# Kernel optimization log

Hardware: AMD Instinct MI355X
Metric: run time of the kernel (lower is better)

Reference implementation:

```python
import jax, jax.numpy as jnp
import numpy as np
import math

DIM = 256
HEADS = 8
HID = DIM * HEADS


def mish(x):
    return x * jnp.tanh(jax.nn.softplus(x))


def setup_inputs() -> dict:
    key = jax.random.key(0)
    ks = jax.random.split(key, 12)
    b, t, l = 4, 16, 256
    s = 1.0 / math.sqrt(DIM)
    inp = {
        "qkv_x": jax.random.normal(ks[0], (b, t, l, DIM), jnp.float32),
        "t_embed": jax.random.normal(ks[1], (b, t, 1, DIM), jnp.float32),
        "reward_embed": jax.random.normal(ks[2], (b, t, 1, DIM), jnp.float32),
        "Wq": jax.random.normal(ks[3], (DIM, HID), jnp.float32) * s,
        "Wk": jax.random.normal(ks[4], (DIM, HID), jnp.float32) * s,
        "Wv": jax.random.normal(ks[5], (DIM, HID), jnp.float32) * s,
        "Wq_t": jax.random.normal(ks[6], (DIM, HID), jnp.float32) * s,
        "bq_t": jnp.zeros((HID,), jnp.float32),
        "Wk_t": jax.random.normal(ks[7], (DIM, HID), jnp.float32) * s,
        "bk_t": jnp.zeros((HID,), jnp.float32),
        "Wv_t": jax.random.normal(ks[8], (DIM, HID), jnp.float32) * s,
        "bv_t": jnp.zeros((HID,), jnp.float32),
        "Wo": jax.random.normal(ks[9], (HID, DIM), jnp.float32) * (1.0 / math.sqrt(HID)),
        "bo": jnp.zeros((DIM,), jnp.float32),
    }
    return inp


def reference(qkv_x, t_embed, reward_embed, Wq, Wk, Wv, Wq_t, bq_t, Wk_t, bk_t, Wv_t, bv_t, Wo, bo):
    b, t, l, f = qkv_x.shape
    x = qkv_x.reshape(b * t, l, f)                    # (bt, l, f)
    tr = (t_embed + reward_embed).reshape(b * t, 1, f)  # (bt, 1, f)
    m = mish(tr)

    def proj(W, Wt, bt_):
        # bias-add of time-conditioning broadcast over l, split heads
        y = x @ W + (m @ Wt + bt_)                    # (bt, l, H*D)
        return y.reshape(b * t, l, HEADS, DIM).transpose(0, 2, 1, 3)  # (bt, H, l, D)

    q = proj(Wq, Wq_t, bq_t)
    k = proj(Wk, Wk_t, bk_t)
    v = proj(Wv, Wv_t, bv_t)

    scores = jnp.einsum('bhqd,bhkd->bhqk', q, k) / math.sqrt(DIM)
    attn = jax.nn.softmax(scores, axis=-1)
    out = jnp.einsum('bhqk,bhkd->bhqd', attn, v)      # (bt, H, l, D)
    out = out.transpose(0, 2, 1, 3).reshape(b, t, l, HEADS * DIM)
    return out @ Wo + bo
```

## Files before the change

kernel.cpp:

```cpp
#include <hip/hip_runtime.h>
#include <stdint.h>

typedef __bf16 bf16x8 __attribute__((ext_vector_type(8)));
typedef float f32x4 __attribute__((ext_vector_type(4)));
typedef uint32_t u32x4 __attribute__((ext_vector_type(4)));

#define MFMA16(a,b,c) __builtin_amdgcn_mfma_f32_16x16x32_bf16(a,b,c,0,0,0)

#define OFF_XB   0ull
#define OFF_WT   8388608ull
#define OFF_WTT  11534336ull
#define OFF_WOT  14680064ull
#define OFF_MB   15728640ull
#define OFF_BIAS 15761408ull
#define OFF_K    17334272ull
#define OFF_VT   84443136ull
#define WS_NEED  151552000ull
#define OFF_Q    151552000ull
#define WS_NEED2 218660864ull

__device__ __forceinline__ uint16_t f2bf(float f) {
  uint32_t u = __builtin_bit_cast(uint32_t, f);
  return (uint16_t)((u + 0x7fffu + ((u >> 16) & 1u)) >> 16);
}
__device__ __forceinline__ bf16x8 ld16(const uint16_t* p) {
  u32x4 v = *(const u32x4*)p;
  return __builtin_bit_cast(bf16x8, v);
}
__device__ __forceinline__ void gll16(const uint16_t* g, char* l) {
  __builtin_amdgcn_global_load_lds(
      (const __attribute__((address_space(1))) void*)g,
      (__attribute__((address_space(3))) void*)l, 16, 0, 0);
}
__device__ __forceinline__ void bounce_w2(char* slab, int row, int col, uint16_t val) {
  int slot = col >> 3;
  *(uint16_t*)(slab + row * 256 + (((slot ^ (row & 7)) & 15) << 4) + ((col & 7) << 1)) = val;
}
__device__ __forceinline__ bf16x8 bounce_r16(const char* slab, int row, int slot) {
  u32x4 v = *(const u32x4*)(slab + row * 256 + (((slot ^ (row & 7)) & 15) << 4));
  return __builtin_bit_cast(bf16x8, v);
}

__global__ void sentinel_kernel(float* out, float val) {
  out[blockIdx.x * 256 + threadIdx.x] = val;
}
__global__ void init_out(const float* bo, float* out) {
  int i = blockIdx.x * 256 + threadIdx.x;
  out[i] = bo[i & 255];
}

__global__ void mish_kernel(const float* te, const float* re, uint16_t* mb) {
  int i = blockIdx.x * 256 + threadIdx.x;
  float x = te[i] + re[i];
  float sp = log1pf(__expf(x));
  mb[i] = f2bf(x * tanhf(sp));
}

__global__ void convx_kernel(const float* x, uint16_t* xb) {
  int i = blockIdx.x * 256 + threadIdx.x;
  float4 v = ((const float4*)x)[i];
  ushort4 o = make_ushort4(f2bf(v.x), f2bf(v.y), f2bf(v.z), f2bf(v.w));
  ((ushort4*)xb)[i] = o;
}

__global__ void wtrans_kernel(const float* w0, const float* w1, const float* w2,
                              const float* w3, const float* w4, const float* w5,
                              const float* w6, uint16_t* wt, uint16_t* wtt, uint16_t* wot) {
  int z = blockIdx.y;
  const float* src; uint16_t* dst; int C;
  if (z < 3)      { src = (z==0)?w0:((z==1)?w1:w2); dst = wt  + (size_t)z*524288;     C=2048; }
  else if (z < 6) { src = (z==3)?w3:((z==4)?w4:w5); dst = wtt + (size_t)(z-3)*524288; C=2048; }
  else            { src = w6; dst = wot;                                              C=256; }
  int R = (z < 6) ? 256 : 2048;
  __shared__ uint16_t tile[32][33];
  int tc = C >> 5;
  int bR = (blockIdx.x / tc) << 5, bC = (blockIdx.x % tc) << 5;
  int tx = threadIdx.x & 31, ty = threadIdx.x >> 5;
  #pragma unroll
  for (int i = 0; i < 4; i++) {
    int r = bR + ty + i * 8;
    tile[ty + i * 8][tx] = f2bf(src[(size_t)r * C + bC + tx]);
  }
  __syncthreads();
  #pragma unroll
  for (int i = 0; i < 4; i++) {
    int c = bC + ty + i * 8;
    dst[(size_t)c * R + bR + tx] = tile[tx][ty + i * 8];
  }
}

__global__ __launch_bounds__(256, 4)
void bias_gemm(const uint16_t* Mb, const uint16_t* WTT,
               const float* bq, const float* bk, const float* bv, float* biasAll) {
  int bid = blockIdx.x;
  int z = bid >> 4, nbt = bid & 15;
  int n0 = nbt << 7;
  const uint16_t* Bsrc = WTT + (size_t)z * 524288;
  const float* bvec = (z == 0) ? bq : ((z == 1) ? bk : bv);
  float* outp = biasAll + (size_t)z * 131072;
  int tid = threadIdx.x, lane = tid & 63, w = tid >> 6;
  int g = lane >> 4, ln = lane & 15;

  bf16x8 af[8];
  #pragma unroll
  for (int ks = 0; ks < 8; ks++)
    af[ks] = ld16(Mb + (size_t)(w*16 + ln) * 256 + ks*32 + g*8);
  f32x4 acc[8];
  #pragma unroll
  for (int j = 0; j < 8; j++) acc[j] = (f32x4){0.f,0.f,0.f,0.f};
  #pragma unroll
  for (int j = 0; j < 8; j++)
    #pragma unroll
    for (int ks = 0; ks < 8; ks++) {
      bf16x8 bf_ = ld16(Bsrc + (size_t)(n0 + j*16 + ln) * 256 + ks*32 + g*8);
      acc[j] = MFMA16(af[ks], bf_, acc[j]);
    }
  #pragma unroll
  for (int j = 0; j < 8; j++) {
    int colg = n0 + j*16 + ln;
    float bb = bvec[colg];
    #pragma unroll
    for (int r = 0; r < 4; r++)
      outp[(size_t)(w*16 + g*4 + r) * 2048 + colg] = acc[j][r] + bb;
  }
}

__global__ __launch_bounds__(256)
void qkv_gemm3(const uint16_t* Xb, const uint16_t* WT, const float* biasAll,
               uint16_t* Kw, uint16_t* Vt, uint16_t* Qw) {
  __shared__ char stage[32768];
  int nwg = gridDim.x, cpx = nwg >> 3;
  int b0 = blockIdx.x;
  int bid = (b0 & 7) * cpx + (b0 >> 3);
  int z2 = bid >> 11, rem = bid & 2047;
  int widx = (z2 + 1) % 3;
  int mb = rem >> 4, nb = rem & 15;
  int m0 = mb << 7, n0 = nb << 7;
  const uint16_t* Bsrc = WT + (size_t)widx * 524288;
  int bt = m0 >> 8;
  const float* bias = biasAll + (size_t)widx * 131072 + (size_t)bt * 2048;
  int tid = threadIdx.x, lane = tid & 63, w = tid >> 6;
  int g = lane >> 4, ln = lane & 15;
  int wr = w >> 1, wc = w & 1;
  int rw = lane >> 3;
  int sg = (lane & 7) ^ rw;

  bool isV = (z2 == 1);
  const char* SA = isV ? stage           : (stage + 16384);
  const char* SB = isV ? (stage + 16384) : stage;
  int RA = isV ? wr*64 : wc*64;
  int RB = isV ? wc*64 : wr*64;

  f32x4 acc[4][4];
  #pragma unroll
  for (int u = 0; u < 4; u++)
    #pragma unroll
    for (int v = 0; v < 4; v++) acc[u][v] = (f32x4){0.f,0.f,0.f,0.f};

  for (int kt = 0; kt < 4; kt++) {
    int k0 = kt << 6;
    __syncthreads();
    #pragma unroll
    for (int c = 0; c < 4; c++) {
      int chunk = w * 4 + c;
      int row = chunk * 8 + rw;
      gll16(Xb   + (size_t)(m0 + row) * 256 + k0 + sg * 8, stage + chunk * 1024);
      gll16(Bsrc + (size_t)(n0 + row) * 256 + k0 + sg * 8, stage + 16384 + chunk * 1024);
    }
    __syncthreads();
    #pragma unroll
    for (int ks = 0; ks < 2; ks++) {
      bf16x8 fa[4], fb[4];
      #pragma unroll
      for (int u = 0; u < 4; u++) {
        int R = RA + u*16 + ln;
        u32x4 x = *(const u32x4*)(SA + R*128 + ((((ks<<2)+g) ^ (R & 7)) << 4));
        fa[u] = __builtin_bit_cast(bf16x8, x);
      }
      #pragma unroll
      for (int v = 0; v < 4; v++) {
        int R = RB + v*16 + ln;
        u32x4 x = *(const u32x4*)(SB + R*128 + ((((ks<<2)+g) ^ (R & 7)) << 4));
        fb[v] = __builtin_bit_cast(bf16x8, x);
      }
      #pragma unroll
      for (int v = 0; v < 4; v++)
        #pragma unroll
        for (int u = 0; u < 4; u++) acc[u][v] = MFMA16(fa[u], fb[v], acc[u][v]);
    }
  }

  int hh = n0 >> 8;
  size_t hb = (size_t)(bt * 8 + hh) << 16;
  int dbase = (n0 & 255) + wc*64;
  int lbase = (m0 & 255) + wr*64;

  if (isV) {
    #pragma unroll
    for (int v = 0; v < 4; v++) {
      float bb = bias[n0 + wc*64 + v*16 + ln];
      int d = dbase + v*16 + ln;
      #pragma unroll
      for (int u = 0; u < 4; u++) {
        int l0 = lbase + u*16 + g*4;
        ushort4 pk = make_ushort4(f2bf(acc[u][v][0]+bb), f2bf(acc[u][v][1]+bb),
                                  f2bf(acc[u][v][2]+bb), f2bf(acc[u][v][3]+bb));
        *(ushort4*)(Vt + hb + ((size_t)d << 8) + l0) = pk;
      }
    }
  } else {
    uint16_t* dst = (z2 == 0) ? Kw : Qw;
    float scale = (z2 == 2) ? 0.0625f : 1.0f;
    #pragma unroll
    for (int u = 0; u < 4; u++) {
      float4 b4 = *(const float4*)(bias + n0 + wc*64 + u*16 + g*4);
      int d0 = dbase + u*16 + g*4;
      #pragma unroll
      for (int v = 0; v < 4; v++) {
        int l = lbase + v*16 + ln;
        ushort4 pk = make_ushort4(f2bf((acc[u][v][0]+b4.x)*scale),
                                  f2bf((acc[u][v][1]+b4.y)*scale),
                                  f2bf((acc[u][v][2]+b4.z)*scale),
                                  f2bf((acc[u][v][3]+b4.w)*scale));
        *(ushort4*)(dst + hb + ((size_t)l << 8) + d0) = pk;
      }
    }
  }
}

__global__ __launch_bounds__(1024, 2)
void attn_core2(const uint16_t* Qw, const uint16_t* Kw, const uint16_t* Vt, uint16_t* Ob) {
  __shared__ char smem[65536];
  int tid = threadIdx.x, lane = tid & 63, w = tid >> 6;
  int g = lane >> 4, ln = lane & 15;
  int bh = blockIdx.x;
  const size_t kvbase = (size_t)bh << 16;
  int q0l = w * 16;
  char* stage = smem;
  char* slab  = smem + 32768 + (w << 11);

  u32x4 rv[2];
  auto issue_tile = [&](const uint16_t* src) {
    #pragma unroll
    for (int it = 0; it < 2; it++) {
      int c = tid + (it << 10);
      int row = c >> 5, sl = c & 31;
      rv[it] = *(const u32x4*)(src + (size_t)row * 256 + sl * 8);
    }
  };
  auto commit_tile = [&]() {
    #pragma unroll
    for (int it = 0; it < 2; it++) {
      int c = tid + (it << 10);
      int row = c >> 5, sl = c & 31;
      *(u32x4*)(stage + row * 512 + ((sl ^ (row & 7)) << 4)) = rv[it];
    }
  };
  auto frag = [&](int row, int slot) -> bf16x8 {
    u32x4 v = *(const u32x4*)(stage + row * 512 + ((slot ^ (row & 7)) << 4));
    return __builtin_bit_cast(bf16x8, v);
  };

  issue_tile(Kw + kvbase);
  bf16x8 qa[8];
  #pragma unroll
  for (int ks = 0; ks < 8; ks++)
    qa[ks] = ld16(Qw + kvbase + (size_t)(q0l + ln) * 256 + ks*32 + g*8);

  f32x4 S[16];
  #pragma unroll
  for (int f = 0; f < 16; f++) S[f] = (f32x4){0.f,0.f,0.f,0.f};
  #pragma unroll
  for (int t = 0; t < 4; t++) {
    __syncthreads();
    commit_tile();
    __syncthreads();
    if (t < 3) issue_tile(Kw + kvbase + (size_t)((t+1)*64) * 256);
    #pragma unroll
    for (int ks = 0; ks < 8; ks++)
      #pragma unroll
      for (int f2 = 0; f2 < 4; f2++)
        S[t*4+f2] = MFMA16(qa[ks], frag(f2*16 + ln, ks*4 + g), S[t*4+f2]);
  }
  issue_tile(Vt + kvbase);

  #pragma unroll
  for (int r = 0; r < 4; r++) {
    float mx = -3.4e38f;
    #pragma unroll
    for (int f = 0; f < 16; f++) mx = fmaxf(mx, S[f][r]);
    #pragma unroll
    for (int m_ = 1; m_ < 16; m_ <<= 1) mx = fmaxf(mx, __shfl_xor(mx, m_, 64));
    float sum = 0.f;
    #pragma unroll
    for (int f = 0; f < 16; f++) {
      float p = __expf(S[f][r] - mx);
      S[f][r] = p; sum += p;
    }
    #pragma unroll
    for (int m_ = 1; m_ < 16; m_ <<= 1) sum += __shfl_xor(sum, m_, 64);
    float inv = 1.f / sum;
    #pragma unroll
    for (int f = 0; f < 16; f++) S[f][r] *= inv;
  }

  bf16x8 pb[8];
  #pragma unroll
  for (int qtr = 0; qtr < 4; qtr++) {
    #pragma unroll
    for (int f2 = 0; f2 < 4; f2++) {
      int col = f2*16 + ln;
      int slot = col >> 3;
      #pragma unroll
      for (int r = 0; r < 4; r++) {
        int row = g*4 + r;
        *(uint16_t*)(slab + row*128 + (((slot ^ (row & 7)) & 7) << 4) + ((col & 7) << 1))
            = f2bf(S[qtr*4+f2][r]);
      }
    }
    #pragma unroll
    for (int i = 0; i < 2; i++) {
      u32x4 v = *(const u32x4*)(slab + ln*128 + ((((i*4+g) ^ (ln & 7)) & 7) << 4));
      pb[qtr*2+i] = __builtin_bit_cast(bf16x8, v);
    }
  }

  f32x4 O[16];
  #pragma unroll
  for (int df = 0; df < 16; df++) O[df] = (f32x4){0.f,0.f,0.f,0.f};
  #pragma unroll
  for (int t = 0; t < 4; t++) {
    __syncthreads();
    commit_tile();
    __syncthreads();
    if (t < 3) issue_tile(Vt + kvbase + (size_t)((t+1)*64) * 256);
    #pragma unroll
    for (int ks = 0; ks < 8; ks++)
      #pragma unroll
      for (int df2 = 0; df2 < 4; df2++)
        O[t*4+df2] = MFMA16(frag(df2*16 + ln, ks*4 + g), pb[ks], O[t*4+df2]);
  }

  size_t obase = kvbase + (size_t)(q0l + ln) * 256;
  #pragma unroll
  for (int df = 0; df < 16; df++) {
    ushort4 pk = make_ushort4(f2bf(O[df][0]), f2bf(O[df][1]), f2bf(O[df][2]), f2bf(O[df][3]));
    *(ushort4*)(Ob + obase + df*16 + g*4) = pk;
  }
}

__global__ __launch_bounds__(256, 4)
void out_gemm(const uint16_t* Ob, const uint16_t* WoT, const float* bo, float* out) {
  __shared__ char stage[16384];
  int bid = blockIdx.x;
  int mt = bid >> 1, nt = bid & 1;
  int m0 = mt << 6, n0 = nt << 7;
  int bt = m0 >> 8;
  int lrow = (m0 & 255);
  int tid = threadIdx.x, lane = tid & 63, w = tid >> 6;
  int g = lane >> 4, ln = lane & 15;

  u32x4 rb[4];
  auto issueW = [&](int kt) {
    #pragma unroll
    for (int it = 0; it < 4; it++) {
      int c = tid + (it << 8);
      int row = c >> 3, sl = c & 7;
      rb[it] = *(const u32x4*)(WoT + (size_t)(n0 + row) * 2048 + kt*64 + sl*8);
    }
  };
  auto aptr = [&](int kt) -> const uint16_t* {
    return Ob + ((size_t)(bt*8 + (kt >> 2)) << 16)
         + (size_t)(lrow + w*16 + ln) * 256 + (kt & 3) * 64;
  };
  issueW(0);
  bf16x8 afc[2];
  { const uint16_t* ab = aptr(0); afc[0] = ld16(ab + g*8); afc[1] = ld16(ab + 32 + g*8); }
  f32x4 acc[8];
  #pragma unroll
  for (int j = 0; j < 8; j++) acc[j] = (f32x4){0.f,0.f,0.f,0.f};

  for (int kt = 0; kt < 32; kt++) {
    __syncthreads();
    #pragma unroll
    for (int it = 0; it < 4; it++) {
      int c = tid + (it << 8);
      int row = c >> 3, sl = c & 7;
      *(u32x4*)(stage + row*128 + (((sl ^ (row & 7)) & 7) << 4)) = rb[it];
    }
    __syncthreads();
    bf16x8 afn[2];
    if (kt < 31) {
      issueW(kt+1);
      const uint16_t* ab = aptr(kt+1);
      afn[0] = ld16(ab + g*8); afn[1] = ld16(ab + 32 + g*8);
    }
    #pragma unroll
    for (int ks = 0; ks < 2; ks++)
      #pragma unroll
      for (int j = 0; j < 8; j++) {
        int row = j*16 + ln;
        u32x4 v = *(const u32x4*)(stage + row*128 + ((((ks*4+g) ^ (row & 7)) & 7) << 4));
        acc[j] = MFMA16(afc[ks], __builtin_bit_cast(bf16x8, v), acc[j]);
      }
    if (kt < 31) { afc[0] = afn[0]; afc[1] = afn[1]; }
  }
  #pragma unroll
  for (int j = 0; j < 8; j++) {
    int col = n0 + j*16 + ln;
    float bb = bo[col];
    #pragma unroll
    for (int r = 0; r < 4; r++)
      out[(size_t)(m0 + w*16 + g*4 + r) * 256 + col] = acc[j][r] + bb;
  }
}

__global__ __launch_bounds__(512, 2)
void attn_v5(const uint16_t* Xb, const uint16_t* WT, const float* Bi,
             const uint16_t* Kw, const uint16_t* Vt, const uint16_t* WoT,
             float* out) {
  __shared__ char smem[65536];
  int tid = threadIdx.x, lane = tid & 63, w = tid >> 6;
  int g = lane >> 4, ln = lane & 15;
  int bid = blockIdx.x;
  int bh = bid >> 1, qh = bid & 1;
  int bt = bh >> 3, h = bh & 7;
  const size_t kvbase = (size_t)bh << 16;
  int q0g = bt * 256 + qh * 128 + w * 16;
  char* stage = smem;
  char* slab  = smem + 32768 + (w << 12);

  u32x4 rv[4];
  auto issue_tile = [&](const uint16_t* src, int rowstride) {
    #pragma unroll
    for (int it = 0; it < 4; it++) {
      int c = tid + (it << 9);
      int row = c >> 5, sl = c & 31;
      rv[it] = *(const u32x4*)(src + (size_t)row * rowstride + sl * 8);
    }
  };
  auto commit_tile = [&]() {
    #pragma unroll
    for (int it = 0; it < 4; it++) {
      int c = tid + (it << 9);
      int row = c >> 5, sl = c & 31;
      *(u32x4*)(stage + row * 512 + ((sl ^ (row & 7)) << 4)) = rv[it];
    }
  };
  auto frag = [&](int row, int slot) -> bf16x8 {
    u32x4 v = *(const u32x4*)(stage + row * 512 + ((slot ^ (row & 7)) << 4));
    return __builtin_bit_cast(bf16x8, v);
  };

  issue_tile(WT + (size_t)(h*256) * 256, 256);
  bf16x8 qx[8];
  #pragma unroll
  for (int ks = 0; ks < 8; ks++)
    qx[ks] = ld16(Xb + (size_t)(q0g + ln) * 256 + ks*32 + g*8);
  f32x4 qacc[16];
  #pragma unroll
  for (int f = 0; f < 16; f++) qacc[f] = (f32x4){0.f,0.f,0.f,0.f};
  #pragma unroll
  for (int t = 0; t < 4; t++) {
    __syncthreads();
    commit_tile();
    __syncthreads();
    if (t < 3) issue_tile(WT + (size_t)(h*256 + (t+1)*64) * 256, 256);
    #pragma unroll
    for (int ks = 0; ks < 8; ks++)
      #pragma unroll
      for (int f2 = 0; f2 < 4; f2++)
        qacc[t*4+f2] = MFMA16(qx[ks], frag(f2*16 + ln, ks*4 + g), qacc[t*4+f2]);
  }
  issue_tile(Kw + kvbase, 256);
  #pragma unroll
  for (int f = 0; f < 16; f++) {
    float bb = Bi[bt*2048 + h*256 + f*16 + ln];
    #pragma unroll
    for (int r = 0; r < 4; r++) qacc[f][r] = (qacc[f][r] + bb) * 0.0625f;
  }
  bf16x8 qa[8];
  #pragma unroll
  for (int dh = 0; dh < 2; dh++) {
    #pragma unroll
    for (int f2 = 0; f2 < 8; f2++) {
      int f = dh*8 + f2;
      #pragma unroll
      for (int r = 0; r < 4; r++)
        bounce_w2(slab, g*4 + r, f2*16 + ln, f2bf(qacc[f][r]));
    }
    #pragma unroll
    for (int ks2 = 0; ks2 < 4; ks2++)
      qa[dh*4 + ks2] = bounce_r16(slab, ln, ks2*4 + g);
  }

  f32x4 S[16];
  #pragma unroll
  for (int f = 0; f < 16; f++) S[f] = (f32x4){0.f,0.f,0.f,0.f};
  #pragma unroll
  for (int t = 0; t < 4; t++) {
    __syncthreads();
    commit_tile();
    __syncthreads();
    if (t < 3) issue_tile(Kw + kvbase + (size_t)((t+1)*64) * 256, 256);
    #pragma unroll
    for (int ks = 0; ks < 8; ks++)
      #pragma unroll
      for (int f2 = 0; f2 < 4; f2++)
        S[t*4+f2] = MFMA16(qa[ks], frag(f2*16 + ln, ks*4 + g), S[t*4+f2]);
  }
  issue_tile(Vt + kvbase, 256);

  #pragma unroll
  for (int r = 0; r < 4; r++) {
    float mx = -3.4e38f;
    #pragma unroll
    for (int f = 0; f < 16; f++) mx = fmaxf(mx, S[f][r]);
    #pragma unroll
    for (int m_ = 1; m_ < 16; m_ <<= 1) mx = fmaxf(mx, __shfl_xor(mx, m_, 64));
    float sum = 0.f;
    #pragma unroll
    for (int f = 0; f < 16; f++) {
      float p = __expf(S[f][r] - mx);
      S[f][r] = p; sum += p;
    }
    #pragma unroll
    for (int m_ = 1; m_ < 16; m_ <<= 1) sum += __shfl_xor(sum, m_, 64);
    float inv = 1.f / sum;
    #pragma unroll
    for (int f = 0; f < 16; f++) S[f][r] *= inv;
  }

  bf16x8 pb[8];
  #pragma unroll
  for (int kh = 0; kh < 2; kh++) {
    #pragma unroll
    for (int f2 = 0; f2 < 8; f2++) {
      int f = kh*8 + f2;
      #pragma unroll
      for (int r = 0; r < 4; r++)
        bounce_w2(slab, g*4 + r, f2*16 + ln, f2bf(S[f][r]));
    }
    #pragma unroll
    for (int ks2 = 0; ks2 < 4; ks2++)
      pb[kh*4 + ks2] = bounce_r16(slab, ln, ks2*4 + g);
  }

  f32x4 O[16];
  #pragma unroll
  for (int df = 0; df < 16; df++) O[df] = (f32x4){0.f,0.f,0.f,0.f};
  #pragma unroll
  for (int t = 0; t < 4; t++) {
    __syncthreads();
    commit_tile();
    __syncthreads();
    if (t < 3) issue_tile(Vt + kvbase + (size_t)((t+1)*64) * 256, 256);
    #pragma unroll
    for (int ks = 0; ks < 8; ks++)
      #pragma unroll
      for (int df2 = 0; df2 < 4; df2++)
        O[t*4+df2] = MFMA16(frag(df2*16 + ln, ks*4 + g), pb[ks], O[t*4+df2]);
  }
  issue_tile(WoT + (size_t)0 * 2048 + h*256, 2048);

  bf16x8 oa[8];
  #pragma unroll
  for (int dh = 0; dh < 2; dh++) {
    #pragma unroll
    for (int df2 = 0; df2 < 8; df2++) {
      int df = dh*8 + df2;
      #pragma unroll
      for (int r = 0; r < 4; r++)
        bounce_w2(slab, ln, df2*16 + g*4 + r, f2bf(O[df][r]));
    }
    #pragma unroll
    for (int ks2 = 0; ks2 < 4; ks2++)
      oa[dh*4 + ks2] = bounce_r16(slab, ln, ks2*4 + g);
  }

  f32x4 oacc[16];
  #pragma unroll
  for (int ef = 0; ef < 16; ef++) oacc[ef] = (f32x4){0.f,0.f,0.f,0.f};
  #pragma unroll
  for (int t = 0; t < 4; t++) {
    __syncthreads();
    commit_tile();
    __syncthreads();
    if (t < 3) issue_tile(WoT + (size_t)((t+1)*64) * 2048 + h*256, 2048);
    #pragma unroll
    for (int ks = 0; ks < 8; ks++)
      #pragma unroll
      for (int ef2 = 0; ef2 < 4; ef2++)
        oacc[t*4+ef2] = MFMA16(oa[ks], frag(ef2*16 + ln, ks*4 + g), oacc[t*4+ef2]);
  }
  #pragma unroll
  for (int ef = 0; ef < 16; ef++)
    #pragma unroll
    for (int r = 0; r < 4; r++)
      atomicAdd(out + (size_t)(q0g + g*4 + r) * 256 + ef*16 + ln, oacc[ef][r]);
}

extern "C" void kernel_launch(void* const* d_in, const int* in_sizes, int n_in,
                              void* d_out, int out_size, void* d_ws, size_t ws_size,
                              hipStream_t stream) {
  float* out = (float*)d_out;
  if (ws_size < WS_NEED) {
    sentinel_kernel<<<16384, 256, 0, stream>>>(out, 1000.0f + (float)(ws_size >> 20));
    return;
  }
  const float* x   = (const float*)d_in[0];
  const float* te  = (const float*)d_in[1];
  const float* re  = (const float*)d_in[2];
  const float* Wq  = (const float*)d_in[3];
  const float* Wk  = (const float*)d_in[4];
  const float* Wv  = (const float*)d_in[5];
  const float* Wqt = (const float*)d_in[6];
  const float* bqt = (const float*)d_in[7];
  const float* Wkt = (const float*)d_in[8];
  const float* bkt = (const float*)d_in[9];
  const float* Wvt = (const float*)d_in[10];
  const float* bvt = (const float*)d_in[11];
  const float* Wo  = (const float*)d_in[12];
  const float* bo  = (const float*)d_in[13];
  char* ws = (char*)d_ws;
  uint16_t* Xb  = (uint16_t*)(ws + OFF_XB);
  uint16_t* WT  = (uint16_t*)(ws + OFF_WT);
  uint16_t* WTT = (uint16_t*)(ws + OFF_WTT);
  uint16_t* WoT = (uint16_t*)(ws + OFF_WOT);
  uint16_t* Mb  = (uint16_t*)(ws + OFF_MB);
  float*    Bi  = (float*)(ws + OFF_BIAS);
  uint16_t* Kw  = (uint16_t*)(ws + OFF_K);
  uint16_t* Vt  = (uint16_t*)(ws + OFF_VT);

  mish_kernel<<<64, 256, 0, stream>>>(te, re, Mb);
  wtrans_kernel<<<dim3(512, 7), 256, 0, stream>>>(Wq, Wk, Wv, Wqt, Wkt, Wvt, Wo, WT, WTT, WoT);
  convx_kernel<<<4096, 256, 0, stream>>>(x, Xb);
  bias_gemm<<<48, 256, 0, stream>>>(Mb, WTT, bqt, bkt, bvt, Bi);

  if (ws_size >= WS_NEED2) {
    uint16_t* Qw = (uint16_t*)(ws + OFF_Q);
    qkv_gemm3<<<6144, 256, 0, stream>>>(Xb, WT, Bi, Kw, Vt, Qw);
    attn_core2<<<512, 1024, 0, stream>>>(Qw, Kw, Vt, Qw);
    out_gemm<<<512, 256, 0, stream>>>(Qw, WoT, bo, out);
  } else {
    qkv_gemm3<<<4096, 256, 0, stream>>>(Xb, WT, Bi, Kw, Vt, Kw);
    init_out<<<16384, 256, 0, stream>>>(bo, out);
    attn_v5<<<1024, 512, 0, stream>>>(Xb, WT, Bi, Kw, Vt, WoT, out);
  }
}
```

Measured before the change: 234.4 us.

## Fuse prep kernels, stage QKV epilogue through LDS, swizzle out_gemm blocks

Merges the mish, x-conversion and weight-transpose kernels into a single launch to cut launch overhead. The QKV GEMM epilogue now writes each wave's tile into swizzled shared memory and then stores 16-byte coalesced rows to K, Q and transposed V, replacing scattered 8-byte stores. out_gemm remaps block ids across 8 groups, likely to spread work over XCDs for cache locality. The costs are an extra barrier and an LDS round trip in the epilogue.

```diff
diff --git a/kernel.cpp b/kernel.cpp
--- a/kernel.cpp
+++ b/kernel.cpp
@@ -49,24 +49,28 @@
   out[i] = bo[i & 255];
 }
 
-__global__ void mish_kernel(const float* te, const float* re, uint16_t* mb) {
-  int i = blockIdx.x * 256 + threadIdx.x;
-  float x = te[i] + re[i];
-  float sp = log1pf(__expf(x));
-  mb[i] = f2bf(x * tanhf(sp));
-}
-
-__global__ void convx_kernel(const float* x, uint16_t* xb) {
-  int i = blockIdx.x * 256 + threadIdx.x;
-  float4 v = ((const float4*)x)[i];
-  ushort4 o = make_ushort4(f2bf(v.x), f2bf(v.y), f2bf(v.z), f2bf(v.w));
-  ((ushort4*)xb)[i] = o;
-}
-
-__global__ void wtrans_kernel(const float* w0, const float* w1, const float* w2,
-                              const float* w3, const float* w4, const float* w5,
-                              const float* w6, uint16_t* wt, uint16_t* wtt, uint16_t* wot) {
-  int z = blockIdx.y;
+__global__ void prep_all(const float* te, const float* re, uint16_t* mb,
+                         const float* x, uint16_t* xb,
+                         const float* w0, const float* w1, const float* w2,
+                         const float* w3, const float* w4, const float* w5,
+                         const float* w6, uint16_t* wt, uint16_t* wtt, uint16_t* wot) {
+  int b = blockIdx.x;
+  if (b < 64) {
+    int i = b * 256 + threadIdx.x;
+    float v = te[i] + re[i];
+    float sp = log1pf(__expf(v));
+    mb[i] = f2bf(v * tanhf(sp));
+    return;
+  }
+  if (b < 4160) {
+    int i = (b - 64) * 256 + threadIdx.x;
+    float4 v = ((const float4*)x)[i];
+    ushort4 o = make_ushort4(f2bf(v.x), f2bf(v.y), f2bf(v.z), f2bf(v.w));
+    ((ushort4*)xb)[i] = o;
+    return;
+  }
+  int local = b - 4160;
+  int z = local >> 9, bx = local & 511;
   const float* src; uint16_t* dst; int C;
   if (z < 3)      { src = (z==0)?w0:((z==1)?w1:w2); dst = wt  + (size_t)z*524288;     C=2048; }
   else if (z < 6) { src = (z==3)?w3:((z==4)?w4:w5); dst = wtt + (size_t)(z-3)*524288; C=2048; }
@@ -74,7 +78,7 @@
   int R = (z < 6) ? 256 : 2048;
   __shared__ uint16_t tile[32][33];
   int tc = C >> 5;
-  int bR = (blockIdx.x / tc) << 5, bC = (blockIdx.x % tc) << 5;
+  int bR = (bx / tc) << 5, bC = (bx % tc) << 5;
   int tx = threadIdx.x & 31, ty = threadIdx.x >> 5;
   #pragma unroll
   for (int i = 0; i < 4; i++) {
@@ -126,7 +130,7 @@
 }
 
 __global__ __launch_bounds__(256)
-void qkv_gemm3(const uint16_t* Xb, const uint16_t* WT, const float* biasAll,
+void qkv_gemm4(const uint16_t* Xb, const uint16_t* WT, const float* biasAll,
                uint16_t* Kw, uint16_t* Vt, uint16_t* Qw) {
   __shared__ char stage[32768];
   int nwg = gridDim.x, cpx = nwg >> 3;
@@ -190,6 +194,8 @@
     }
   }
 
+  __syncthreads();
+  char* esl = stage + (w << 13);
   int hh = n0 >> 8;
   size_t hb = (size_t)(bt * 8 + hh) << 16;
   int dbase = (n0 & 255) + wc*64;
@@ -199,31 +205,44 @@
     #pragma unroll
     for (int v = 0; v < 4; v++) {
       float bb = bias[n0 + wc*64 + v*16 + ln];
-      int d = dbase + v*16 + ln;
+      int row = v*16 + ln;
       #pragma unroll
       for (int u = 0; u < 4; u++) {
-        int l0 = lbase + u*16 + g*4;
+        int col0 = u*16 + g*4;
         ushort4 pk = make_ushort4(f2bf(acc[u][v][0]+bb), f2bf(acc[u][v][1]+bb),
                                   f2bf(acc[u][v][2]+bb), f2bf(acc[u][v][3]+bb));
-        *(ushort4*)(Vt + hb + ((size_t)d << 8) + l0) = pk;
+        *(ushort4*)(esl + row*128 + ((((col0 >> 3) ^ (row & 7)) & 7) << 4)
+                    + ((col0 & 7) << 1)) = pk;
       }
     }
   } else {
-    uint16_t* dst = (z2 == 0) ? Kw : Qw;
     float scale = (z2 == 2) ? 0.0625f : 1.0f;
     #pragma unroll
     for (int u = 0; u < 4; u++) {
       float4 b4 = *(const float4*)(bias + n0 + wc*64 + u*16 + g*4);
-      int d0 = dbase + u*16 + g*4;
       #pragma unroll
       for (int v = 0; v < 4; v++) {
-        int l = lbase + v*16 + ln;
+        int row = v*16 + ln;
+        int col0 = u*16 + g*4;
         ushort4 pk = make_ushort4(f2bf((acc[u][v][0]+b4.x)*scale),
                                   f2bf((acc[u][v][1]+b4.y)*scale),
                                   f2bf((acc[u][v][2]+b4.z)*scale),
                                   f2bf((acc[u][v][3]+b4.w)*scale));
-        *(ushort4*)(dst + hb + ((size_t)l << 8) + d0) = pk;
+        *(ushort4*)(esl + row*128 + ((((col0 >> 3) ^ (row & 7)) & 7) << 4)
+                    + ((col0 & 7) << 1)) = pk;
       }
+    }
+  }
+  #pragma unroll
+  for (int it = 0; it < 8; it++) {
+    int idx = it*64 + lane;
+    int row = idx >> 3, ch = idx & 7;
+    u32x4 v = *(const u32x4*)(esl + row*128 + (((ch ^ (row & 7)) & 7) << 4));
+    if (isV) {
+      *(u32x4*)(Vt + hb + ((size_t)(dbase + row) << 8) + lbase + ch*8) = v;
+    } else {
+      uint16_t* dst = (z2 == 0) ? Kw : Qw;
+      *(u32x4*)(dst + hb + ((size_t)(lbase + row) << 8) + dbase + ch*8) = v;
     }
   }
 }
@@ -352,7 +371,8 @@
 __global__ __launch_bounds__(256, 4)
 void out_gemm(const uint16_t* Ob, const uint16_t* WoT, const float* bo, float* out) {
   __shared__ char stage[16384];
-  int bid = blockIdx.x;
+  int b0 = blockIdx.x;
+  int bid = (b0 & 7) * 64 + (b0 >> 3);
   int mt = bid >> 1, nt = bid & 1;
   int m0 = mt << 6, n0 = nt << 7;
   int bt = m0 >> 8;
@@ -632,18 +652,17 @@
   uint16_t* Kw  = (uint16_t*)(ws + OFF_K);
   uint16_t* Vt  = (uint16_t*)(ws + OFF_VT);
 
-  mish_kernel<<<64, 256, 0, stream>>>(te, re, Mb);
-  wtrans_kernel<<<dim3(512, 7), 256, 0, stream>>>(Wq, Wk, Wv, Wqt, Wkt, Wvt, Wo, WT, WTT, WoT);
-  convx_kernel<<<4096, 256, 0, stream>>>(x, Xb);
+  prep_all<<<7744, 256, 0, stream>>>(te, re, Mb, x, Xb,
+                                     Wq, Wk, Wv, Wqt, Wkt, Wvt, Wo, WT, WTT, WoT);
   bias_gemm<<<48, 256, 0, stream>>>(Mb, WTT, bqt, bkt, bvt, Bi);
 
   if (ws_size >= WS_NEED2) {
     uint16_t* Qw = (uint16_t*)(ws + OFF_Q);
-    qkv_gemm3<<<6144, 256, 0, stream>>>(Xb, WT, Bi, Kw, Vt, Qw);
+    qkv_gemm4<<<6144, 256, 0, stream>>>(Xb, WT, Bi, Kw, Vt, Qw);
     attn_core2<<<512, 1024, 0, stream>>>(Qw, Kw, Vt, Qw);
     out_gemm<<<512, 256, 0, stream>>>(Qw, WoT, bo, out);
   } else {
-    qkv_gemm3<<<4096, 256, 0, stream>>>(Xb, WT, Bi, Kw, Vt, Kw);
+    qkv_gemm4<<<4096, 256, 0, stream>>>(Xb, WT, Bi, Kw, Vt, Kw);
     init_out<<<16384, 256, 0, stream>>>(bo, out);
     attn_v5<<<1024, 512, 0, stream>>>(Xb, WT, Bi, Kw, Vt, WoT, out);
   }
```

Measured after the change: 207.1 us, median of 2. -11.7%, faster.
